# Performance work log

Measured on AMD Instinct MI355X. Metric: run time of the kernel, lower is better.

The kernel has to match this reference:

```python
import jax, jax.numpy as jnp
import numpy as np

# dims: batch, d_features(m), n_subsets, sub_size(k=ceil(m/n)), heads, d_k, d_v, conv kernel, d_out
B, M, N, K, H, DK, DV, KER, D = 512, 4096, 64, 64, 8, 32, 4, 3, 4096
DOUT_PER = D // N  # d_out_per_subset = 64
EPS_LN = 1e-5      # torch nn.LayerNorm default eps


def setup_inputs() -> dict:
    key = jax.random.key(0)
    ks = jax.random.split(key, 8)
    s = 0.02  # xavier-like scale
    return {
        "features": jax.random.normal(ks[0], (B, M), dtype=jnp.float32),
        # per-head permutation of the m feature indices (f_shuffle(m, h, seeds))
        "shuffled_index": jnp.argsort(jax.random.uniform(ks[1], (H, M)), axis=1).astype(jnp.int32),
        "gamma": jnp.ones((M,), jnp.float32),
        "beta": jnp.zeros((M,), jnp.float32),
        "W_q": (jax.random.normal(ks[2], (H * DK, K)) * s).astype(jnp.float32),   # Linear(k, h*d_k)
        "W_k": (jax.random.normal(ks[3], (H, DK, K)) * s).astype(jnp.float32),    # grouped Conv1d(h, h*d_k, kernel=k, stride=k)
        "W_v1": (jax.random.normal(ks[4], (H, DV, KER)) * s).astype(jnp.float32), # grouped Conv1d(h, h*d_v, kernel)
        "W_v2": (jax.random.normal(ks[5], (H, DV)) * s).astype(jnp.float32),      # grouped Conv1d(h*d_v, h, 1)
        "W_fc": (jax.random.normal(ks[6], (DOUT_PER, H * K)) * s).astype(jnp.float32),
    }


def reference(features, shuffled_index, gamma, beta, W_q, W_k, W_v1, W_v2, W_fc):
    b = features.shape[0]
    # LayerNorm over m (query path only)
    mu = features.mean(-1, keepdims=True)
    var = ((features - mu) ** 2).mean(-1, keepdims=True)
    q_in = (features - mu) / jnp.sqrt(var + EPS_LN) * gamma + beta

    # shuffled gather: [b, H, M]  (k*n == m here so k_pad/q_pad are no-ops)
    sf = features[:, shuffled_index]

    # query: [b, n, k] -> Linear(k, h*d_k) -> [b, H, N, DK]
    q = jnp.einsum('bnk,ek->bne', q_in.reshape(b, N, K), W_q)
    q = q.reshape(b, N, H, DK).transpose(0, 2, 1, 3)

    # key: grouped conv kernel=stride=k == per-subset contraction -> [b, H, DK, N]
    kf = sf.reshape(b, H, N, K)
    key_ = jnp.einsum('bhnk,hdk->bhdn', kf, W_k)

    # value: [b, N, H, K], right-pad by KER-1, depthwise conv -> relu -> 1x1 conv -> +residual
    v = kf.transpose(0, 2, 1, 3)  # [b, N, H, K]
    vp = jnp.pad(v, ((0, 0), (0, 0), (0, 0), (0, KER - 1)))
    win = jnp.stack([vp[..., t:t + K] for t in range(KER)], axis=-1)  # [b,N,H,K,KER]
    v1 = jnp.einsum('bnhpt,hdt->bnhdp', win, W_v1)
    v2 = jnp.einsum('bnhdp,hd->bnhp', jax.nn.relu(v1), W_v2)
    v = (v2 + v).transpose(0, 2, 1, 3)  # [b, H, N, K]

    # scaled dot-product attention, temperature = sqrt(m)
    attn = jax.nn.softmax(jnp.einsum('bhqd,bhdk->bhqk', q, key_) / jnp.sqrt(jnp.float32(M)), axis=-1)
    out = jnp.einsum('bhqk,bhks->bhqs', attn, v)           # [b, H, N, K]
    out = out.transpose(0, 2, 1, 3).reshape(b, N, H * K)   # [b, N, H*K]
    out = jnp.einsum('bnf,of->bno', out, W_fc).reshape(b, N * DOUT_PER)
    return out, attn.reshape(b * H, N, N)
```

## Files before the change

kernel.cpp:

```cpp
#include <hip/hip_runtime.h>

typedef __bf16 v8bf __attribute__((ext_vector_type(8)));
typedef __bf16 v4bf __attribute__((ext_vector_type(4)));
typedef __bf16 v2bf __attribute__((ext_vector_type(2)));
typedef float  v4f  __attribute__((ext_vector_type(4)));

namespace {

constexpr int kB = 512, kM = 4096, kH = 8;

constexpr size_t WS_QIN = 0;
constexpr size_t WS_O   = (size_t)4 << 20;
constexpr size_t WS_WQ  = WS_O + (size_t)32768 * 512 * 2;
constexpr size_t WS_WK  = WS_WQ + 32768;
constexpr size_t WS_WFC = WS_WK + 32768;


__global__ __launch_bounds__(256) void k0_weights(
    const float* __restrict__ Wq, const float* __restrict__ Wk,
    const float* __restrict__ Wfc,
    __bf16* __restrict__ wq, __bf16* __restrict__ wk, __bf16* __restrict__ wfc) {
  int i = blockIdx.x * 256 + threadIdx.x;
  if (i < 16384) {
    int e = i >> 6, k = i & 63;
    int dst = ((e >> 4) * 2 + (k >> 5)) * 512 + (e & 15) * 32 + (k & 31);
    wq[dst] = (__bf16)(Wq[i] * 0.015625f);
  } else if (i < 32768) {
    int j = i - 16384;
    int e = j >> 6, k = j & 63;
    int dst = ((e >> 4) * 2 + (k >> 5)) * 512 + (e & 15) * 32 + (k & 31);
    wk[dst] = (__bf16)Wk[j];
  } else {
    int j = i - 32768;
    int o = j >> 9, f = j & 511;
    int dst = ((o >> 4) * 16 + (f >> 5)) * 512 + (o & 15) * 32 + (f & 31);
    wfc[dst] = (__bf16)Wfc[j];
  }
}

__global__ __launch_bounds__(256) void k1_ln(
    const float* __restrict__ feat, const float* __restrict__ gamma,
    const float* __restrict__ beta, __bf16* __restrict__ qin) {
  __shared__ float red[4];
  const int b = blockIdx.x, t = threadIdx.x, lane = t & 63, wv = t >> 6;
  const float* frow = feat + (size_t)b * kM;
  float xs[16];
  float s = 0.f;
#pragma unroll
  for (int j = 0; j < 16; ++j) { float x = frow[t + j * 256]; xs[j] = x; s += x; }
#pragma unroll
  for (int o = 32; o > 0; o >>= 1) s += __shfl_xor(s, o);
  if (lane == 0) red[wv] = s;
  __syncthreads();
  const float mu = (red[0] + red[1] + red[2] + red[3]) * (1.f / kM);
  float v = 0.f;
#pragma unroll
  for (int j = 0; j < 16; ++j) { float d = xs[j] - mu; v += d * d; }
#pragma unroll
  for (int o = 32; o > 0; o >>= 1) v += __shfl_xor(v, o);
  __syncthreads();
  if (lane == 0) red[wv] = v;
  __syncthreads();
  const float var  = (red[0] + red[1] + red[2] + red[3]) * (1.f / kM);
  const float rstd = rsqrtf(var + 1e-5f);
#pragma unroll
  for (int j = 0; j < 16; ++j) {
    int m = t + j * 256;
    int n = m >> 6, k = m & 63;
    int dst = ((n >> 4) * 2 + (k >> 5)) * 512 + (n & 15) * 32 + (k & 31);
    qin[(size_t)b * kM + dst] = (__bf16)((xs[j] - mu) * rstd * gamma[m] + beta[m]);
  }
}

__global__ __launch_bounds__(256, 4) void k2_attn(
    const float* __restrict__ feat, const int* __restrict__ sidx,
    const __bf16* __restrict__ qin, const __bf16* __restrict__ wq,
    const __bf16* __restrict__ wk, const float* __restrict__ Wv1,
    const float* __restrict__ Wv2, __bf16* __restrict__ o_ws,
    float* __restrict__ out) {
  __shared__ __align__(16) __bf16 smem[18432];
  __bf16* s_feat = smem;
  __bf16* s_kf   = smem + 4096;
  __bf16* s_q    = smem + 8704;
  __bf16* s_K    = smem + 11264;
  __bf16* s_vT   = smem + 13824;
  __bf16* s_sc   = smem + 4096;

  const int b = blockIdx.x, h = blockIdx.y;
  const int t = threadIdx.x, w = t >> 6, lid = t & 63;
  const int quad = lid >> 4, l16 = lid & 15;

  const float*  frow  = feat + (size_t)b * kM;
  const int*    idxh  = sidx + h * kM;
  const __bf16* qin_b = qin + (size_t)b * kM;
  float* attn_out = out + (size_t)kB * kM + ((size_t)(b * kH + h)) * 4096;

  int idxr[16];
#pragma unroll
  for (int j = 0; j < 16; ++j) idxr[j] = idxh[t + j * 256];

  {
    const float4* frow4 = reinterpret_cast<const float4*>(frow);
#pragma unroll
    for (int j = 0; j < 4; ++j) {
      int i4 = t + j * 256;
      float4 f = frow4[i4];
      v4bf o4;
      o4[0] = (__bf16)f.x; o4[1] = (__bf16)f.y; o4[2] = (__bf16)f.z; o4[3] = (__bf16)f.w;
      *(v4bf*)(s_feat + 4 * i4) = o4;
    }
  }

  if (t < 64) {
    v8bf z = {};
    *(v8bf*)(s_kf + t * 72 + 64) = z;
  }

  v4f dq0 = {0.f, 0.f, 0.f, 0.f}, dq1 = {0.f, 0.f, 0.f, 0.f};
#pragma unroll
  for (int kt = 0; kt < 2; ++kt) {
    v8bf a  = *(const v8bf*)(qin_b + (2 * w + kt) * 512 + l16 * 32 + 8 * quad);
    v8bf b0 = *(const v8bf*)(wq + (size_t)(4 * h + kt) * 512 + l16 * 32 + 8 * quad);
    v8bf b1 = *(const v8bf*)(wq + (size_t)(4 * h + 2 + kt) * 512 + l16 * 32 + 8 * quad);
    dq0 = __builtin_amdgcn_mfma_f32_16x16x32_bf16(a, b0, dq0, 0, 0, 0);
    dq1 = __builtin_amdgcn_mfma_f32_16x16x32_bf16(a, b1, dq1, 0, 0, 0);
  }
#pragma unroll
  for (int r = 0; r < 4; ++r) {
    s_q[(16 * w + 4 * quad + r) * 40 + l16]      = (__bf16)dq0[r];
    s_q[(16 * w + 4 * quad + r) * 40 + 16 + l16] = (__bf16)dq1[r];
  }

  __syncthreads();

#pragma unroll
  for (int j = 0; j < 16; ++j) {
    int i = t + j * 256;
    s_kf[(i >> 6) * 72 + (i & 63)] = s_feat[idxr[j]];
  }

  __syncthreads();

  {
    v4f dk0 = {0.f, 0.f, 0.f, 0.f}, dk1 = {0.f, 0.f, 0.f, 0.f};
#pragma unroll
    for (int kt = 0; kt < 2; ++kt) {
      v8bf a  = *(const v8bf*)(s_kf + (16 * w + l16) * 72 + 32 * kt + 8 * quad);
      v8bf b0 = *(const v8bf*)(wk + (size_t)(4 * h + kt) * 512 + l16 * 32 + 8 * quad);
      v8bf b1 = *(const v8bf*)(wk + (size_t)(4 * h + 2 + kt) * 512 + l16 * 32 + 8 * quad);
      dk0 = __builtin_amdgcn_mfma_f32_16x16x32_bf16(a, b0, dk0, 0, 0, 0);
      dk1 = __builtin_amdgcn_mfma_f32_16x16x32_bf16(a, b1, dk1, 0, 0, 0);
    }
#pragma unroll
    for (int r = 0; r < 4; ++r) {
      s_K[(16 * w + 4 * quad + r) * 40 + l16]      = (__bf16)dk0[r];
      s_K[(16 * w + 4 * quad + r) * 40 + 16 + l16] = (__bf16)dk1[r];
    }
  }

  {
    const int n = t & 63, p0 = (t >> 6) * 16;
    float w1[4][3], w2[4];
#pragma unroll
    for (int d = 0; d < 4; ++d) {
#pragma unroll
      for (int c = 0; c < 3; ++c) w1[d][c] = Wv1[(h * 4 + d) * 3 + c];
      w2[d] = Wv2[h * 4 + d];
    }
    v8bf xa = *(const v8bf*)(s_kf + n * 72 + p0);
    v8bf xb = *(const v8bf*)(s_kf + n * 72 + p0 + 8);
    v2bf xc = *(const v2bf*)(s_kf + n * 72 + p0 + 16);
    float x[18];
#pragma unroll
    for (int c = 0; c < 8; ++c) { x[c] = (float)xa[c]; x[c + 8] = (float)xb[c]; }
    x[16] = (float)xc[0]; x[17] = (float)xc[1];
#pragma unroll
    for (int pp = 0; pp < 16; ++pp) {
      float acc = x[pp];
#pragma unroll
      for (int d = 0; d < 4; ++d) {
        float v1 = fmaf(x[pp + 2], w1[d][2], fmaf(x[pp + 1], w1[d][1], x[pp] * w1[d][0]));
        acc = fmaf(fmaxf(v1, 0.f), w2[d], acc);
      }
      s_vT[(p0 + pp) * 72 + n] = (__bf16)acc;
    }
  }

  __syncthreads();

  {
    v4f ds[4] = {{0.f, 0.f, 0.f, 0.f}, {0.f, 0.f, 0.f, 0.f},
                 {0.f, 0.f, 0.f, 0.f}, {0.f, 0.f, 0.f, 0.f}};
    v8bf a = *(const v8bf*)(s_q + (16 * w + l16) * 40 + 8 * quad);
#pragma unroll
    for (int nt = 0; nt < 4; ++nt) {
      v8bf bb = *(const v8bf*)(s_K + (16 * nt + l16) * 40 + 8 * quad);
      ds[nt] = __builtin_amdgcn_mfma_f32_16x16x32_bf16(a, bb, ds[nt], 0, 0, 0);
    }
#pragma unroll
    for (int nt = 0; nt < 4; ++nt)
#pragma unroll
      for (int r = 0; r < 4; ++r)
        s_sc[(16 * w + 4 * quad + r) * 72 + 16 * nt + l16] = (__bf16)ds[nt][r];
  }

#pragma unroll
  for (int rr = 0; rr < 4; ++rr) {
    const int row = 16 * w + 4 * rr + quad;
    v4bf pv = *(const v4bf*)(s_sc + row * 72 + 4 * l16);
    float e0 = (float)pv[0], e1 = (float)pv[1], e2 = (float)pv[2], e3 = (float)pv[3];
    float mx = fmaxf(fmaxf(e0, e1), fmaxf(e2, e3));
#pragma unroll
    for (int mk = 8; mk > 0; mk >>= 1) mx = fmaxf(mx, __shfl_xor(mx, mk));
    e0 = __expf(e0 - mx); e1 = __expf(e1 - mx);
    e2 = __expf(e2 - mx); e3 = __expf(e3 - mx);
    float ssum = e0 + e1 + e2 + e3;
#pragma unroll
    for (int mk = 8; mk > 0; mk >>= 1) ssum += __shfl_xor(ssum, mk);
    const float inv = 1.0f / ssum;
    e0 *= inv; e1 *= inv; e2 *= inv; e3 *= inv;
    *(float4*)(attn_out + row * 64 + 4 * l16) = make_float4(e0, e1, e2, e3);
    v4bf st;
    st[0] = (__bf16)e0; st[1] = (__bf16)e1; st[2] = (__bf16)e2; st[3] = (__bf16)e3;
    *(v4bf*)(s_sc + row * 72 + 4 * l16) = st;
  }

  v4f dO[4] = {{0.f, 0.f, 0.f, 0.f}, {0.f, 0.f, 0.f, 0.f},
               {0.f, 0.f, 0.f, 0.f}, {0.f, 0.f, 0.f, 0.f}};
#pragma unroll
  for (int kt = 0; kt < 2; ++kt) {
    v8bf a = *(const v8bf*)(s_sc + (16 * w + l16) * 72 + 32 * kt + 8 * quad);
#pragma unroll
    for (int st = 0; st < 4; ++st) {
      v8bf bb = *(const v8bf*)(s_vT + (16 * st + l16) * 72 + 32 * kt + 8 * quad);
      dO[st] = __builtin_amdgcn_mfma_f32_16x16x32_bf16(a, bb, dO[st], 0, 0, 0);
    }
  }

  __bf16* obase = o_ws + ((size_t)(b * 4 + w) * 16 + h * 2) * 512;
#pragma unroll
  for (int st = 0; st < 4; ++st)
#pragma unroll
    for (int r = 0; r < 4; ++r)
      obase[(st >> 1) * 512 + (4 * quad + r) * 32 + (st & 1) * 16 + l16] = (__bf16)dO[st][r];
}

__global__ __launch_bounds__(256, 4) void k3_fc(
    const __bf16* __restrict__ o_ws, const __bf16* __restrict__ wfc,
    float* __restrict__ out) {
  const int t = threadIdx.x, w = t >> 6, lid = t & 63;
  const int quad = lid >> 4, l16 = lid & 15;
  const size_t row0 = (size_t)blockIdx.x * 64 + 16 * w;
  const __bf16* abase = o_ws + (size_t)(blockIdx.x * 4 + w) * 16 * 512;
  v4f d[4] = {{0.f, 0.f, 0.f, 0.f}, {0.f, 0.f, 0.f, 0.f},
              {0.f, 0.f, 0.f, 0.f}, {0.f, 0.f, 0.f, 0.f}};
#pragma unroll 4
  for (int kt = 0; kt < 16; ++kt) {
    v8bf a = *(const v8bf*)(abase + kt * 512 + l16 * 32 + 8 * quad);
#pragma unroll
    for (int nt = 0; nt < 4; ++nt) {
      v8bf bb = *(const v8bf*)(wfc + (size_t)(nt * 16 + kt) * 512 + l16 * 32 + 8 * quad);
      d[nt] = __builtin_amdgcn_mfma_f32_16x16x32_bf16(a, bb, d[nt], 0, 0, 0);
    }
  }
#pragma unroll
  for (int nt = 0; nt < 4; ++nt)
#pragma unroll
    for (int r = 0; r < 4; ++r)
      out[(row0 + 4 * quad + r) * 64 + 16 * nt + l16] = d[nt][r];
}

}

extern "C" void kernel_launch(void* const* d_in, const int* in_sizes, int n_in,
                              void* d_out, int out_size, void* d_ws, size_t ws_size,
                              hipStream_t stream) {
  (void)in_sizes; (void)n_in; (void)out_size; (void)ws_size;
  const float* features = (const float*)d_in[0];
  const int*   sidx     = (const int*)d_in[1];
  const float* gamma    = (const float*)d_in[2];
  const float* beta     = (const float*)d_in[3];
  const float* Wq       = (const float*)d_in[4];
  const float* Wk       = (const float*)d_in[5];
  const float* Wv1      = (const float*)d_in[6];
  const float* Wv2      = (const float*)d_in[7];
  const float* Wfc      = (const float*)d_in[8];
  float* out = (float*)d_out;

  char* ws = (char*)d_ws;
  __bf16* ws_qin = (__bf16*)(ws + WS_QIN);
  __bf16* ws_o   = (__bf16*)(ws + WS_O);
  __bf16* ws_wq  = (__bf16*)(ws + WS_WQ);
  __bf16* ws_wk  = (__bf16*)(ws + WS_WK);
  __bf16* ws_wfc = (__bf16*)(ws + WS_WFC);

  hipLaunchKernelGGL(k0_weights, dim3(256), dim3(256), 0, stream,
                     Wq, Wk, Wfc, ws_wq, ws_wk, ws_wfc);
  hipLaunchKernelGGL(k1_ln, dim3(kB), dim3(256), 0, stream,
                     features, gamma, beta, ws_qin);
  hipLaunchKernelGGL(k2_attn, dim3(kB, kH), dim3(256), 0, stream,
                     features, sidx, ws_qin, ws_wq, ws_wk, Wv1, Wv2, ws_o, out);
  hipLaunchKernelGGL(k3_fc, dim3(kB), dim3(256), 0, stream,
                     ws_o, ws_wfc, out);
}
```

Measured before the change: 152.0 us.

## Fuse layernorm, per-head attention and FC projection into one per-batch kernel

```diff
diff --git a/kernel.cpp b/kernel.cpp
--- a/kernel.cpp
+++ b/kernel.cpp
@@ -8,12 +8,6 @@
 namespace {
 
 constexpr int kB = 512, kM = 4096, kH = 8;
-
-constexpr size_t WS_QIN = 0;
-constexpr size_t WS_O   = (size_t)4 << 20;
-constexpr size_t WS_WQ  = WS_O + (size_t)32768 * 512 * 2;
-constexpr size_t WS_WK  = WS_WQ + 32768;
-constexpr size_t WS_WFC = WS_WK + 32768;
 
 
 __global__ __launch_bounds__(256) void k0_weights(
@@ -38,236 +32,238 @@
   }
 }
 
-__global__ __launch_bounds__(256) void k1_ln(
-    const float* __restrict__ feat, const float* __restrict__ gamma,
-    const float* __restrict__ beta, __bf16* __restrict__ qin) {
+__global__ __launch_bounds__(256, 2) void k_fused(
+    const float* __restrict__ feat, const int* __restrict__ sidx,
+    const float* __restrict__ gamma, const float* __restrict__ beta,
+    const __bf16* __restrict__ wq, const __bf16* __restrict__ wk,
+    const float* __restrict__ Wv1, const float* __restrict__ Wv2,
+    const __bf16* __restrict__ wfc, float* __restrict__ out) {
+  __shared__ __align__(16) __bf16 smem[26624];
   __shared__ float red[4];
-  const int b = blockIdx.x, t = threadIdx.x, lane = t & 63, wv = t >> 6;
-  const float* frow = feat + (size_t)b * kM;
-  float xs[16];
+  __bf16* s_feat = smem;
+  __bf16* s_qin  = smem + 4096;
+  __bf16* s_kf   = smem + 8192;
+  __bf16* s_q    = smem + 12800;
+  __bf16* s_K    = smem + 15360;
+  __bf16* s_vT   = smem + 17920;
+  __bf16* s_o    = smem + 22528;
+  __bf16* s_sc   = s_kf;
+
+  const int b = blockIdx.x;
+  const int t = threadIdx.x, w = t >> 6, lane = t & 63;
+  const int quad = lane >> 4, l16 = lane & 15;
+
+  const float4* frow4 = reinterpret_cast<const float4*>(feat + (size_t)b * kM);
+  const float4* g4  = reinterpret_cast<const float4*>(gamma);
+  const float4* be4 = reinterpret_cast<const float4*>(beta);
+  float4 xs[4];
   float s = 0.f;
 #pragma unroll
-  for (int j = 0; j < 16; ++j) { float x = frow[t + j * 256]; xs[j] = x; s += x; }
+  for (int j = 0; j < 4; ++j) {
+    xs[j] = frow4[t + j * 256];
+    s += xs[j].x + xs[j].y + xs[j].z + xs[j].w;
+  }
+  int idxr[16], idxn[16];
+#pragma unroll
+  for (int j = 0; j < 16; ++j) idxr[j] = sidx[t + j * 256];
 #pragma unroll
   for (int o = 32; o > 0; o >>= 1) s += __shfl_xor(s, o);
-  if (lane == 0) red[wv] = s;
+  if (lane == 0) red[w] = s;
   __syncthreads();
   const float mu = (red[0] + red[1] + red[2] + red[3]) * (1.f / kM);
-  float v = 0.f;
-#pragma unroll
-  for (int j = 0; j < 16; ++j) { float d = xs[j] - mu; v += d * d; }
-#pragma unroll
-  for (int o = 32; o > 0; o >>= 1) v += __shfl_xor(v, o);
-  __syncthreads();
-  if (lane == 0) red[wv] = v;
+  float var_p = 0.f;
+#pragma unroll
+  for (int j = 0; j < 4; ++j) {
+    float d0 = xs[j].x - mu, d1 = xs[j].y - mu, d2 = xs[j].z - mu, d3 = xs[j].w - mu;
+    var_p += d0 * d0 + d1 * d1 + d2 * d2 + d3 * d3;
+  }
+#pragma unroll
+  for (int o = 32; o > 0; o >>= 1) var_p += __shfl_xor(var_p, o);
+  __syncthreads();
+  if (lane == 0) red[w] = var_p;
   __syncthreads();
   const float var  = (red[0] + red[1] + red[2] + red[3]) * (1.f / kM);
   const float rstd = rsqrtf(var + 1e-5f);
 #pragma unroll
-  for (int j = 0; j < 16; ++j) {
-    int m = t + j * 256;
-    int n = m >> 6, k = m & 63;
-    int dst = ((n >> 4) * 2 + (k >> 5)) * 512 + (n & 15) * 32 + (k & 31);
-    qin[(size_t)b * kM + dst] = (__bf16)((xs[j] - mu) * rstd * gamma[m] + beta[m]);
-  }
-}
-
-__global__ __launch_bounds__(256, 4) void k2_attn(
-    const float* __restrict__ feat, const int* __restrict__ sidx,
-    const __bf16* __restrict__ qin, const __bf16* __restrict__ wq,
-    const __bf16* __restrict__ wk, const float* __restrict__ Wv1,
-    const float* __restrict__ Wv2, __bf16* __restrict__ o_ws,
-    float* __restrict__ out) {
-  __shared__ __align__(16) __bf16 smem[18432];
-  __bf16* s_feat = smem;
-  __bf16* s_kf   = smem + 4096;
-  __bf16* s_q    = smem + 8704;
-  __bf16* s_K    = smem + 11264;
-  __bf16* s_vT   = smem + 13824;
-  __bf16* s_sc   = smem + 4096;
-
-  const int b = blockIdx.x, h = blockIdx.y;
-  const int t = threadIdx.x, w = t >> 6, lid = t & 63;
-  const int quad = lid >> 4, l16 = lid & 15;
-
-  const float*  frow  = feat + (size_t)b * kM;
-  const int*    idxh  = sidx + h * kM;
-  const __bf16* qin_b = qin + (size_t)b * kM;
-  float* attn_out = out + (size_t)kB * kM + ((size_t)(b * kH + h)) * 4096;
-
-  int idxr[16];
-#pragma unroll
-  for (int j = 0; j < 16; ++j) idxr[j] = idxh[t + j * 256];
-
-  {
-    const float4* frow4 = reinterpret_cast<const float4*>(frow);
-#pragma unroll
-    for (int j = 0; j < 4; ++j) {
-      int i4 = t + j * 256;
-      float4 f = frow4[i4];
-      v4bf o4;
-      o4[0] = (__bf16)f.x; o4[1] = (__bf16)f.y; o4[2] = (__bf16)f.z; o4[3] = (__bf16)f.w;
-      *(v4bf*)(s_feat + 4 * i4) = o4;
-    }
-  }
-
-  if (t < 64) {
-    v8bf z = {};
-    *(v8bf*)(s_kf + t * 72 + 64) = z;
-  }
-
-  v4f dq0 = {0.f, 0.f, 0.f, 0.f}, dq1 = {0.f, 0.f, 0.f, 0.f};
-#pragma unroll
-  for (int kt = 0; kt < 2; ++kt) {
-    v8bf a  = *(const v8bf*)(qin_b + (2 * w + kt) * 512 + l16 * 32 + 8 * quad);
-    v8bf b0 = *(const v8bf*)(wq + (size_t)(4 * h + kt) * 512 + l16 * 32 + 8 * quad);
-    v8bf b1 = *(const v8bf*)(wq + (size_t)(4 * h + 2 + kt) * 512 + l16 * 32 + 8 * quad);
-    dq0 = __builtin_amdgcn_mfma_f32_16x16x32_bf16(a, b0, dq0, 0, 0, 0);
-    dq1 = __builtin_amdgcn_mfma_f32_16x16x32_bf16(a, b1, dq1, 0, 0, 0);
-  }
-#pragma unroll
-  for (int r = 0; r < 4; ++r) {
-    s_q[(16 * w + 4 * quad + r) * 40 + l16]      = (__bf16)dq0[r];
-    s_q[(16 * w + 4 * quad + r) * 40 + 16 + l16] = (__bf16)dq1[r];
-  }
-
-  __syncthreads();
-
-#pragma unroll
-  for (int j = 0; j < 16; ++j) {
-    int i = t + j * 256;
-    s_kf[(i >> 6) * 72 + (i & 63)] = s_feat[idxr[j]];
-  }
-
-  __syncthreads();
-
-  {
-    v4f dk0 = {0.f, 0.f, 0.f, 0.f}, dk1 = {0.f, 0.f, 0.f, 0.f};
+  for (int j = 0; j < 4; ++j) {
+    const int i4 = t + j * 256;
+    float4 g = g4[i4], bt = be4[i4];
+    v4bf fb, qb;
+    fb[0] = (__bf16)xs[j].x; fb[1] = (__bf16)xs[j].y;
+    fb[2] = (__bf16)xs[j].z; fb[3] = (__bf16)xs[j].w;
+    qb[0] = (__bf16)((xs[j].x - mu) * rstd * g.x + bt.x);
+    qb[1] = (__bf16)((xs[j].y - mu) * rstd * g.y + bt.y);
+    qb[2] = (__bf16)((xs[j].z - mu) * rstd * g.z + bt.z);
+    qb[3] = (__bf16)((xs[j].w - mu) * rstd * g.w + bt.w);
+    *(v4bf*)(s_feat + 4 * i4) = fb;
+    const int n = (t >> 4) + 16 * j, k = 4 * (t & 15);
+    const int dst = ((n >> 4) * 2 + (k >> 5)) * 512 + (n & 15) * 32 + (k & 31);
+    *(v4bf*)(s_qin + dst) = qb;
+  }
+  if (t < 64) { v8bf z = {}; *(v8bf*)(s_kf + t * 72 + 64) = z; }
+  __syncthreads();
+
+  v4f acc[4] = {{0.f, 0.f, 0.f, 0.f}, {0.f, 0.f, 0.f, 0.f},
+                {0.f, 0.f, 0.f, 0.f}, {0.f, 0.f, 0.f, 0.f}};
+
+  for (int h = 0; h < kH; ++h) {
+    {
+      v4f dq0 = {0.f, 0.f, 0.f, 0.f}, dq1 = {0.f, 0.f, 0.f, 0.f};
+#pragma unroll
+      for (int kt = 0; kt < 2; ++kt) {
+        v8bf a  = *(const v8bf*)(s_qin + (2 * w + kt) * 512 + l16 * 32 + 8 * quad);
+        v8bf b0 = *(const v8bf*)(wq + (size_t)(4 * h + kt) * 512 + l16 * 32 + 8 * quad);
+        v8bf b1 = *(const v8bf*)(wq + (size_t)(4 * h + 2 + kt) * 512 + l16 * 32 + 8 * quad);
+        dq0 = __builtin_amdgcn_mfma_f32_16x16x32_bf16(a, b0, dq0, 0, 0, 0);
+        dq1 = __builtin_amdgcn_mfma_f32_16x16x32_bf16(a, b1, dq1, 0, 0, 0);
+      }
+#pragma unroll
+      for (int r = 0; r < 4; ++r) {
+        s_q[(16 * w + 4 * quad + r) * 40 + l16]      = (__bf16)dq0[r];
+        s_q[(16 * w + 4 * quad + r) * 40 + 16 + l16] = (__bf16)dq1[r];
+      }
+    }
+
+    if (h < kH - 1) {
+      const int* idxp = sidx + (h + 1) * kM;
+#pragma unroll
+      for (int j = 0; j < 16; ++j) idxn[j] = idxp[t + j * 256];
+    }
+
+#pragma unroll
+    for (int j = 0; j < 16; ++j) {
+      int i = t + j * 256;
+      s_kf[(i >> 6) * 72 + (i & 63)] = s_feat[idxr[j]];
+    }
+    __syncthreads();
+
+    {
+      v4f dk0 = {0.f, 0.f, 0.f, 0.f}, dk1 = {0.f, 0.f, 0.f, 0.f};
+#pragma unroll
+      for (int kt = 0; kt < 2; ++kt) {
+        v8bf a  = *(const v8bf*)(s_kf + (16 * w + l16) * 72 + 32 * kt + 8 * quad);
+        v8bf b0 = *(const v8bf*)(wk + (size_t)(4 * h + kt) * 512 + l16 * 32 + 8 * quad);
+        v8bf b1 = *(const v8bf*)(wk + (size_t)(4 * h + 2 + kt) * 512 + l16 * 32 + 8 * quad);
+        dk0 = __builtin_amdgcn_mfma_f32_16x16x32_bf16(a, b0, dk0, 0, 0, 0);
+        dk1 = __builtin_amdgcn_mfma_f32_16x16x32_bf16(a, b1, dk1, 0, 0, 0);
+      }
+#pragma unroll
+      for (int r = 0; r < 4; ++r) {
+        s_K[(16 * w + 4 * quad + r) * 40 + l16]      = (__bf16)dk0[r];
+        s_K[(16 * w + 4 * quad + r) * 40 + 16 + l16] = (__bf16)dk1[r];
+      }
+    }
+
+    {
+      const int n = t & 63, p0 = (t >> 6) * 16;
+      float w1[4][3], w2[4];
+#pragma unroll
+      for (int d = 0; d < 4; ++d) {
+#pragma unroll
+        for (int c = 0; c < 3; ++c) w1[d][c] = Wv1[(h * 4 + d) * 3 + c];
+        w2[d] = Wv2[h * 4 + d];
+      }
+      v8bf xa = *(const v8bf*)(s_kf + n * 72 + p0);
+      v8bf xb = *(const v8bf*)(s_kf + n * 72 + p0 + 8);
+      v2bf xc = *(const v2bf*)(s_kf + n * 72 + p0 + 16);
+      float x[18];
+#pragma unroll
+      for (int c = 0; c < 8; ++c) { x[c] = (float)xa[c]; x[c + 8] = (float)xb[c]; }
+      x[16] = (float)xc[0]; x[17] = (float)xc[1];
+#pragma unroll
+      for (int pp = 0; pp < 16; ++pp) {
+        float a0 = x[pp];
+#pragma unroll
+        for (int d = 0; d < 4; ++d) {
+          float v1 = fmaf(x[pp + 2], w1[d][2], fmaf(x[pp + 1], w1[d][1], x[pp] * w1[d][0]));
+          a0 = fmaf(fmaxf(v1, 0.f), w2[d], a0);
+        }
+        s_vT[(p0 + pp) * 72 + n] = (__bf16)a0;
+      }
+    }
+    __syncthreads();
+
+    {
+      v4f ds[4] = {{0.f, 0.f, 0.f, 0.f}, {0.f, 0.f, 0.f, 0.f},
+                   {0.f, 0.f, 0.f, 0.f}, {0.f, 0.f, 0.f, 0.f}};
+      v8bf a = *(const v8bf*)(s_q + (16 * w + l16) * 40 + 8 * quad);
+#pragma unroll
+      for (int nt = 0; nt < 4; ++nt) {
+        v8bf bb = *(const v8bf*)(s_K + (16 * nt + l16) * 40 + 8 * quad);
+        ds[nt] = __builtin_amdgcn_mfma_f32_16x16x32_bf16(a, bb, ds[nt], 0, 0, 0);
+      }
+#pragma unroll
+      for (int nt = 0; nt < 4; ++nt)
+#pragma unroll
+        for (int r = 0; r < 4; ++r)
+          s_sc[(16 * w + 4 * quad + r) * 72 + 16 * nt + l16] = (__bf16)ds[nt][r];
+    }
+
+    float* attn_out = out + (size_t)kB * kM + ((size_t)(b * kH + h)) * 4096;
+#pragma unroll
+    for (int rr = 0; rr < 4; ++rr) {
+      const int row = 16 * w + 4 * rr + quad;
+      v4bf pv = *(const v4bf*)(s_sc + row * 72 + 4 * l16);
+      float e0 = (float)pv[0], e1 = (float)pv[1], e2 = (float)pv[2], e3 = (float)pv[3];
+      float mx = fmaxf(fmaxf(e0, e1), fmaxf(e2, e3));
+#pragma unroll
+      for (int mk = 8; mk > 0; mk >>= 1) mx = fmaxf(mx, __shfl_xor(mx, mk));
+      e0 = __expf(e0 - mx); e1 = __expf(e1 - mx);
+      e2 = __expf(e2 - mx); e3 = __expf(e3 - mx);
+      float ssum = e0 + e1 + e2 + e3;
+#pragma unroll
+      for (int mk = 8; mk > 0; mk >>= 1) ssum += __shfl_xor(ssum, mk);
+      const float inv = 1.0f / ssum;
+      e0 *= inv; e1 *= inv; e2 *= inv; e3 *= inv;
+      *(float4*)(attn_out + row * 64 + 4 * l16) = make_float4(e0, e1, e2, e3);
+      v4bf st;
+      st[0] = (__bf16)e0; st[1] = (__bf16)e1; st[2] = (__bf16)e2; st[3] = (__bf16)e3;
+      *(v4bf*)(s_sc + row * 72 + 4 * l16) = st;
+    }
+
+    v4f dO[4] = {{0.f, 0.f, 0.f, 0.f}, {0.f, 0.f, 0.f, 0.f},
+                 {0.f, 0.f, 0.f, 0.f}, {0.f, 0.f, 0.f, 0.f}};
 #pragma unroll
     for (int kt = 0; kt < 2; ++kt) {
-      v8bf a  = *(const v8bf*)(s_kf + (16 * w + l16) * 72 + 32 * kt + 8 * quad);
-      v8bf b0 = *(const v8bf*)(wk + (size_t)(4 * h + kt) * 512 + l16 * 32 + 8 * quad);
-      v8bf b1 = *(const v8bf*)(wk + (size_t)(4 * h + 2 + kt) * 512 + l16 * 32 + 8 * quad);
-      dk0 = __builtin_amdgcn_mfma_f32_16x16x32_bf16(a, b0, dk0, 0, 0, 0);
-      dk1 = __builtin_amdgcn_mfma_f32_16x16x32_bf16(a, b1, dk1, 0, 0, 0);
-    }
-#pragma unroll
-    for (int r = 0; r < 4; ++r) {
-      s_K[(16 * w + 4 * quad + r) * 40 + l16]      = (__bf16)dk0[r];
-      s_K[(16 * w + 4 * quad + r) * 40 + 16 + l16] = (__bf16)dk1[r];
-    }
-  }
-
-  {
-    const int n = t & 63, p0 = (t >> 6) * 16;
-    float w1[4][3], w2[4];
-#pragma unroll
-    for (int d = 0; d < 4; ++d) {
-#pragma unroll
-      for (int c = 0; c < 3; ++c) w1[d][c] = Wv1[(h * 4 + d) * 3 + c];
-      w2[d] = Wv2[h * 4 + d];
-    }
-    v8bf xa = *(const v8bf*)(s_kf + n * 72 + p0);
-    v8bf xb = *(const v8bf*)(s_kf + n * 72 + p0 + 8);
-    v2bf xc = *(const v2bf*)(s_kf + n * 72 + p0 + 16);
-    float x[18];
-#pragma unroll
-    for (int c = 0; c < 8; ++c) { x[c] = (float)xa[c]; x[c + 8] = (float)xb[c]; }
-    x[16] = (float)xc[0]; x[17] = (float)xc[1];
-#pragma unroll
-    for (int pp = 0; pp < 16; ++pp) {
-      float acc = x[pp];
-#pragma unroll
-      for (int d = 0; d < 4; ++d) {
-        float v1 = fmaf(x[pp + 2], w1[d][2], fmaf(x[pp + 1], w1[d][1], x[pp] * w1[d][0]));
-        acc = fmaf(fmaxf(v1, 0.f), w2[d], acc);
-      }
-      s_vT[(p0 + pp) * 72 + n] = (__bf16)acc;
-    }
-  }
-
-  __syncthreads();
-
-  {
-    v4f ds[4] = {{0.f, 0.f, 0.f, 0.f}, {0.f, 0.f, 0.f, 0.f},
-                 {0.f, 0.f, 0.f, 0.f}, {0.f, 0.f, 0.f, 0.f}};
-    v8bf a = *(const v8bf*)(s_q + (16 * w + l16) * 40 + 8 * quad);
-#pragma unroll
-    for (int nt = 0; nt < 4; ++nt) {
-      v8bf bb = *(const v8bf*)(s_K + (16 * nt + l16) * 40 + 8 * quad);
-      ds[nt] = __builtin_amdgcn_mfma_f32_16x16x32_bf16(a, bb, ds[nt], 0, 0, 0);
-    }
-#pragma unroll
-    for (int nt = 0; nt < 4; ++nt)
-#pragma unroll
-      for (int r = 0; r < 4; ++r)
-        s_sc[(16 * w + 4 * quad + r) * 72 + 16 * nt + l16] = (__bf16)ds[nt][r];
-  }
-
-#pragma unroll
-  for (int rr = 0; rr < 4; ++rr) {
-    const int row = 16 * w + 4 * rr + quad;
-    v4bf pv = *(const v4bf*)(s_sc + row * 72 + 4 * l16);
-    float e0 = (float)pv[0], e1 = (float)pv[1], e2 = (float)pv[2], e3 = (float)pv[3];
-    float mx = fmaxf(fmaxf(e0, e1), fmaxf(e2, e3));
-#pragma unroll
-    for (int mk = 8; mk > 0; mk >>= 1) mx = fmaxf(mx, __shfl_xor(mx, mk));
-    e0 = __expf(e0 - mx); e1 = __expf(e1 - mx);
-    e2 = __expf(e2 - mx); e3 = __expf(e3 - mx);
-    float ssum = e0 + e1 + e2 + e3;
-#pragma unroll
-    for (int mk = 8; mk > 0; mk >>= 1) ssum += __shfl_xor(ssum, mk);
-    const float inv = 1.0f / ssum;
-    e0 *= inv; e1 *= inv; e2 *= inv; e3 *= inv;
-    *(float4*)(attn_out + row * 64 + 4 * l16) = make_float4(e0, e1, e2, e3);
-    v4bf st;
-    st[0] = (__bf16)e0; st[1] = (__bf16)e1; st[2] = (__bf16)e2; st[3] = (__bf16)e3;
-    *(v4bf*)(s_sc + row * 72 + 4 * l16) = st;
-  }
-
-  v4f dO[4] = {{0.f, 0.f, 0.f, 0.f}, {0.f, 0.f, 0.f, 0.f},
-               {0.f, 0.f, 0.f, 0.f}, {0.f, 0.f, 0.f, 0.f}};
-#pragma unroll
-  for (int kt = 0; kt < 2; ++kt) {
-    v8bf a = *(const v8bf*)(s_sc + (16 * w + l16) * 72 + 32 * kt + 8 * quad);
-#pragma unroll
-    for (int st = 0; st < 4; ++st) {
-      v8bf bb = *(const v8bf*)(s_vT + (16 * st + l16) * 72 + 32 * kt + 8 * quad);
-      dO[st] = __builtin_amdgcn_mfma_f32_16x16x32_bf16(a, bb, dO[st], 0, 0, 0);
-    }
-  }
-
-  __bf16* obase = o_ws + ((size_t)(b * 4 + w) * 16 + h * 2) * 512;
-#pragma unroll
-  for (int st = 0; st < 4; ++st)
+      v8bf a = *(const v8bf*)(s_sc + (16 * w + l16) * 72 + 32 * kt + 8 * quad);
+#pragma unroll
+      for (int st = 0; st < 4; ++st) {
+        v8bf bb = *(const v8bf*)(s_vT + (16 * st + l16) * 72 + 32 * kt + 8 * quad);
+        dO[st] = __builtin_amdgcn_mfma_f32_16x16x32_bf16(a, bb, dO[st], 0, 0, 0);
+      }
+    }
+
+    {
+      __bf16* ob = s_o + w * 1024;
+#pragma unroll
+      for (int st = 0; st < 4; ++st)
+#pragma unroll
+        for (int r = 0; r < 4; ++r)
+          ob[(st >> 1) * 512 + (4 * quad + r) * 32 + (st & 1) * 16 + l16] = (__bf16)dO[st][r];
+#pragma unroll
+      for (int kt = 0; kt < 2; ++kt) {
+        v8bf a = *(const v8bf*)(ob + kt * 512 + l16 * 32 + 8 * quad);
+#pragma unroll
+        for (int nt = 0; nt < 4; ++nt) {
+          v8bf bb = *(const v8bf*)(wfc + (size_t)(nt * 16 + h * 2 + kt) * 512 + l16 * 32 + 8 * quad);
+          acc[nt] = __builtin_amdgcn_mfma_f32_16x16x32_bf16(a, bb, acc[nt], 0, 0, 0);
+        }
+      }
+    }
+    __syncthreads();
+
+    if (h < kH - 1) {
+#pragma unroll
+      for (int j = 0; j < 16; ++j) idxr[j] = idxn[j];
+    }
+  }
+
+  float* orow = out + (size_t)b * kM;
+#pragma unroll
+  for (int nt = 0; nt < 4; ++nt)
 #pragma unroll
     for (int r = 0; r < 4; ++r)
-      obase[(st >> 1) * 512 + (4 * quad + r) * 32 + (st & 1) * 16 + l16] = (__bf16)dO[st][r];
-}
-
-__global__ __launch_bounds__(256, 4) void k3_fc(
-    const __bf16* __restrict__ o_ws, const __bf16* __restrict__ wfc,
-    float* __restrict__ out) {
-  const int t = threadIdx.x, w = t >> 6, lid = t & 63;
-  const int quad = lid >> 4, l16 = lid & 15;
-  const size_t row0 = (size_t)blockIdx.x * 64 + 16 * w;
-  const __bf16* abase = o_ws + (size_t)(blockIdx.x * 4 + w) * 16 * 512;
-  v4f d[4] = {{0.f, 0.f, 0.f, 0.f}, {0.f, 0.f, 0.f, 0.f},
-              {0.f, 0.f, 0.f, 0.f}, {0.f, 0.f, 0.f, 0.f}};
-#pragma unroll 4
-  for (int kt = 0; kt < 16; ++kt) {
-    v8bf a = *(const v8bf*)(abase + kt * 512 + l16 * 32 + 8 * quad);
-#pragma unroll
-    for (int nt = 0; nt < 4; ++nt) {
-      v8bf bb = *(const v8bf*)(wfc + (size_t)(nt * 16 + kt) * 512 + l16 * 32 + 8 * quad);
-      d[nt] = __builtin_amdgcn_mfma_f32_16x16x32_bf16(a, bb, d[nt], 0, 0, 0);
-    }
-  }
-#pragma unroll
-  for (int nt = 0; nt < 4; ++nt)
-#pragma unroll
-    for (int r = 0; r < 4; ++r)
-      out[(row0 + 4 * quad + r) * 64 + 16 * nt + l16] = d[nt][r];
+      orow[(16 * w + 4 * quad + r) * 64 + 16 * nt + l16] = acc[nt][r];
 }
 
 }
@@ -288,18 +284,12 @@
   float* out = (float*)d_out;
 
   char* ws = (char*)d_ws;
-  __bf16* ws_qin = (__bf16*)(ws + WS_QIN);
-  __bf16* ws_o   = (__bf16*)(ws + WS_O);
-  __bf16* ws_wq  = (__bf16*)(ws + WS_WQ);
-  __bf16* ws_wk  = (__bf16*)(ws + WS_WK);
-  __bf16* ws_wfc = (__bf16*)(ws + WS_WFC);
+  __bf16* ws_wq  = (__bf16*)(ws);
+  __bf16* ws_wk  = (__bf16*)(ws + 32768);
+  __bf16* ws_wfc = (__bf16*)(ws + 65536);
 
   hipLaunchKernelGGL(k0_weights, dim3(256), dim3(256), 0, stream,
                      Wq, Wk, Wfc, ws_wq, ws_wk, ws_wfc);
-  hipLaunchKernelGGL(k1_ln, dim3(kB), dim3(256), 0, stream,
-                     features, gamma, beta, ws_qin);
-  hipLaunchKernelGGL(k2_attn, dim3(kB, kH), dim3(256), 0, stream,
-                     features, sidx, ws_qin, ws_wq, ws_wk, Wv1, Wv2, ws_o, out);
-  hipLaunchKernelGGL(k3_fc, dim3(kB), dim3(256), 0, stream,
-                     ws_o, ws_wfc, out);
-}
+  hipLaunchKernelGGL(k_fused, dim3(kB), dim3(256), 0, stream,
+                     features, sidx, gamma, beta, ws_wq, ws_wk, Wv1, Wv2, ws_wfc, out);
+}
```

Measured after the change: 137.3 us. 1.11x faster.
